# Performance work log

Hardware: AMD Instinct MI355X
Metric: run time of the kernel (lower is better)

The kernel has to match this reference:

```python
import jax, jax.numpy as jnp
import numpy as np

D_MODEL = 1024
NUM_HEADS = 16
D_K = D_MODEL // NUM_HEADS


def setup_inputs() -> dict:
    key = jax.random.key(0)
    ks = jax.random.split(key, 11)
    B, S, D = 2, 2048, D_MODEL
    s = 1.0 / np.sqrt(D)  # torch Linear default init scale
    inp = {
        'query': jax.random.normal(ks[0], (B, S, D), jnp.float32),
        'key': jax.random.normal(ks[1], (B, S, D), jnp.float32),
        'value': jax.random.normal(ks[2], (B, S, D), jnp.float32),
        'Wq': jax.random.uniform(ks[3], (D, D), jnp.float32, -s, s),
        'bq': jax.random.uniform(ks[4], (D,), jnp.float32, -s, s),
        'Wk': jax.random.uniform(ks[5], (D, D), jnp.float32, -s, s),
        'bk': jax.random.uniform(ks[6], (D,), jnp.float32, -s, s),
        'Wv': jax.random.uniform(ks[7], (D, D), jnp.float32, -s, s),
        'bv': jax.random.uniform(ks[8], (D,), jnp.float32, -s, s),
        'Wo': jax.random.uniform(ks[9], (D, D), jnp.float32, -s, s),
        'bo': jax.random.uniform(ks[10], (D,), jnp.float32, -s, s),
    }
    return inp


def reference(query, key, value, Wq, bq, Wk, bk, Wv, bv, Wo, bo):
    B, S, D = query.shape
    H, dk = NUM_HEADS, D_K
    # Linear projections (torch Linear: x @ W.T + b), split into heads -> [B,H,S,dk]
    Q = (query @ Wq.T + bq).reshape(B, S, H, dk).transpose(0, 2, 1, 3)
    K = (key @ Wk.T + bk).reshape(B, S, H, dk).transpose(0, 2, 1, 3)
    V = (value @ Wv.T + bv).reshape(B, S, H, dk).transpose(0, 2, 1, 3)
    scale = jnp.sqrt(jnp.asarray(dk, query.dtype))
    scores = jnp.einsum('bhqd,bhkd->bhqk', Q, K) / scale  # [B,H,S,S]
    attn = jax.nn.softmax(scores, axis=-1)
    ctx = jnp.einsum('bhqk,bhkd->bhqd', attn, V)  # [B,H,S,dk]
    ctx = ctx.transpose(0, 2, 1, 3).reshape(B, S, D)
    return ctx @ Wo.T + bo
```

## Files before the change

kernel.cpp:

```cpp
#include <hip/hip_runtime.h>

#define SEQ 2048
#define DM  1024
#define NH  16
#define DK  64
#define BATCH 2
#define MROWS (BATCH * SEQ)
#define PPITCH 72

typedef __attribute__((ext_vector_type(8))) short bf16x8;
typedef __attribute__((ext_vector_type(4))) float f32x4;

__device__ __forceinline__ float bf2f(unsigned short u) {
    union { unsigned int i; float f; } v;
    v.i = ((unsigned int)u) << 16;
    return v.f;
}

__device__ __forceinline__ unsigned short f2bf(float f) {
    union { float f; unsigned int i; } v;
    v.f = f;
    unsigned int r = v.i + 0x7FFFu + ((v.i >> 16) & 1u);
    return (unsigned short)(r >> 16);
}

__device__ __forceinline__ uint4 pack8(float4 x, float4 y) {
    uint4 r;
    r.x = (unsigned)f2bf(x.x) | ((unsigned)f2bf(x.y) << 16);
    r.y = (unsigned)f2bf(x.z) | ((unsigned)f2bf(x.w) << 16);
    r.z = (unsigned)f2bf(y.x) | ((unsigned)f2bf(y.y) << 16);
    r.w = (unsigned)f2bf(y.z) | ((unsigned)f2bf(y.w) << 16);
    return r;
}

__device__ __forceinline__ void gll16(const void* g, void* l) {
    __builtin_amdgcn_global_load_lds(
        (const __attribute__((address_space(1))) unsigned int*)g,
        (__attribute__((address_space(3))) unsigned int*)l, 16, 0, 0);
}

__global__ void detect_dtype(const unsigned short* __restrict__ q,
                             unsigned int* __restrict__ flag) {
    const int lane = threadIdx.x;
    unsigned short u = q[lane * 2];
    int e = (u >> 7) & 0xFF;
    int hit = (e >= 100 && e <= 135) ? 1 : 0;
    unsigned long long m = __ballot(hit);
    if (lane == 0) *flag = (__popcll(m) >= 48) ? 0u : 1u;
}

#define CVT_TOTAL 16781312u
struct CvtArgs {
    const void* src[11];
    unsigned short* dst[11];
};

__global__ __launch_bounds__(256) void convert_all(CvtArgs a,
                                                   const unsigned int* __restrict__ flagp) {
    const unsigned int f = *flagp;
    const size_t e0 = ((size_t)blockIdx.x * 256 + threadIdx.x) * 8;
    if (e0 >= CVT_TOTAL) return;
    const unsigned int cum[12] = {0u, 4194304u, 8388608u, 12582912u, 13631488u,
                                  14680064u, 15728640u, 16777216u, 16778240u,
                                  16779264u, 16780288u, 16781312u};
    int r = 0;
    #pragma unroll
    for (int i = 1; i < 11; ++i) r += (e0 >= cum[i]) ? 1 : 0;
    const size_t local = e0 - cum[r];
    if (f) {
        const float* s = (const float*)a.src[r] + local;
        float4 x = *(const float4*)s;
        float4 y = *(const float4*)(s + 4);
        *(uint4*)(a.dst[r] + local) = pack8(x, y);
    } else {
        *(uint4*)(a.dst[r] + local) =
            *(const uint4*)((const unsigned short*)a.src[r] + local);
    }
}

__device__ __forceinline__ void gemm_core(
    const unsigned short* __restrict__ A, const unsigned short* __restrict__ W,
    const unsigned short* __restrict__ bias, void* __restrict__ C, int cMode)
{
    __shared__ unsigned short Al[128 * 64];
    __shared__ unsigned short Bl[128 * 64];

    const int tid  = threadIdx.x;
    const int w    = tid >> 6;
    const int lane = tid & 63;
    const int lo   = lane & 15;
    const int quad = lane >> 4;
    const int wr   = w >> 1;
    const int wc   = w & 1;
    const int bm   = blockIdx.y * 128;
    const int bn   = blockIdx.x * 128;

    const int r8  = lane >> 3;
    const int csw = ((lane ^ r8) & 7) * 8;
    const unsigned short* gA = A + (size_t)(bm + w * 32 + r8) * DM + csw;
    const unsigned short* gB = W + (size_t)(bn + w * 32 + r8) * DM + csw;
    unsigned short* lA = &Al[(w * 32) * 64];
    unsigned short* lB = &Bl[(w * 32) * 64];

    f32x4 acc[4][4];
    #pragma unroll
    for (int i = 0; i < 4; ++i)
        #pragma unroll
        for (int n = 0; n < 4; ++n) acc[i][n] = (f32x4){0.f, 0.f, 0.f, 0.f};

    const int swz = (lo & 7);

    for (int k0 = 0; k0 < DM; k0 += 64) {
        __syncthreads();
        #pragma unroll
        for (int j = 0; j < 4; ++j) {
            gll16(gA + (size_t)j * 8 * DM + k0, lA + j * 8 * 64);
            gll16(gB + (size_t)j * 8 * DM + k0, lB + j * 8 * 64);
        }
        __syncthreads();

        #pragma unroll
        for (int kc = 0; kc < 2; ++kc) {
            bf16x8 af[4], bfr[4];
            #pragma unroll
            for (int i = 0; i < 4; ++i)
                af[i] = *(const bf16x8*)&Al[(wr * 64 + i * 16 + lo) * 64 +
                                            (((kc * 4 + quad) ^ swz) * 8)];
            #pragma unroll
            for (int n = 0; n < 4; ++n)
                bfr[n] = *(const bf16x8*)&Bl[(wc * 64 + n * 16 + lo) * 64 +
                                             (((kc * 4 + quad) ^ swz) * 8)];
            #pragma unroll
            for (int i = 0; i < 4; ++i)
                #pragma unroll
                for (int n = 0; n < 4; ++n)
                    acc[i][n] = __builtin_amdgcn_mfma_f32_16x16x32_bf16(af[i], bfr[n], acc[i][n], 0, 0, 0);
        }
    }

    float bj[4];
    #pragma unroll
    for (int n = 0; n < 4; ++n)
        bj[n] = bf2f(bias[bn + wc * 64 + n * 16 + lo]);

    if (cMode == 2) {
        #pragma unroll
        for (int i = 0; i < 4; ++i)
            #pragma unroll
            for (int n = 0; n < 4; ++n) {
                const int row0 = bm + wr * 64 + i * 16 + quad * 4;
                const int col  = bn + wc * 64 + n * 16 + lo;
                ushort4 cv;
                cv.x = f2bf(acc[i][n][0] + bj[n]);
                cv.y = f2bf(acc[i][n][1] + bj[n]);
                cv.z = f2bf(acc[i][n][2] + bj[n]);
                cv.w = f2bf(acc[i][n][3] + bj[n]);
                const size_t off = ((size_t)((row0 >> 11) * 16 + (col >> 6)) * 64
                                    + (col & 63)) * 2048 + (row0 & 2047);
                *(ushort4*)((unsigned short*)C + off) = cv;
            }
    } else {
        #pragma unroll
        for (int i = 0; i < 4; ++i)
            #pragma unroll
            for (int n = 0; n < 4; ++n)
                #pragma unroll
                for (int r = 0; r < 4; ++r) {
                    const int row = bm + wr * 64 + i * 16 + quad * 4 + r;
                    const size_t off = (size_t)row * DM + bn + wc * 64 + n * 16 + lo;
                    const float vv = acc[i][n][r] + bj[n];
                    if (cMode == 1) ((float*)C)[off] = vv;
                    else            ((unsigned short*)C)[off] = f2bf(vv);
                }
    }
}

__global__ __launch_bounds__(256) void gemm_qkv(
    const unsigned short* __restrict__ qa, const unsigned short* __restrict__ ka,
    const unsigned short* __restrict__ va,
    const unsigned short* __restrict__ wq, const unsigned short* __restrict__ wk,
    const unsigned short* __restrict__ wv,
    const unsigned short* __restrict__ bq, const unsigned short* __restrict__ bk,
    const unsigned short* __restrict__ bv,
    unsigned short* __restrict__ oq, unsigned short* __restrict__ ok,
    unsigned short* __restrict__ ovT)
{
    if (blockIdx.z == 0)      gemm_core(qa, wq, bq, oq, 0);
    else if (blockIdx.z == 1) gemm_core(ka, wk, bk, ok, 0);
    else                      gemm_core(va, wv, bv, ovT, 2);
}

__global__ __launch_bounds__(256) void gemm_out(
    const unsigned short* __restrict__ A, const unsigned short* __restrict__ W,
    const unsigned short* __restrict__ B, void* __restrict__ C,
    const unsigned int* __restrict__ flagp)
{
    gemm_core(A, W, B, C, (int)*flagp);
}

__global__ __launch_bounds__(256) void attn_mfma2(
    const unsigned short* __restrict__ Q,
    const unsigned short* __restrict__ K,
    const unsigned short* __restrict__ VT,
    unsigned short* __restrict__ CTX)
{
    __shared__ unsigned short Kl[64 * 64];
    __shared__ unsigned short Vl[64 * 64];
    __shared__ unsigned short Pl[4][2][16 * PPITCH];

    const int tid  = threadIdx.x;
    const int w    = tid >> 6;
    const int lane = tid & 63;
    const int lo   = lane & 15;
    const int quad = lane >> 4;
    const int bh = blockIdx.y;
    const int b  = bh >> 4;
    const int h  = bh & 15;
    const int q0 = blockIdx.x * 128 + w * 32;

    bf16x8 aq[2][2];
    #pragma unroll
    for (int f = 0; f < 2; ++f)
        #pragma unroll
        for (int c = 0; c < 2; ++c)
            aq[f][c] = *(const bf16x8*)(Q + (size_t)(b * SEQ + q0 + f * 16 + lo) * DM
                                        + h * 64 + c * 32 + quad * 8);

    f32x4 o[2][4];
    #pragma unroll
    for (int f = 0; f < 2; ++f)
        #pragma unroll
        for (int dt = 0; dt < 4; ++dt) o[f][dt] = (f32x4){0.f, 0.f, 0.f, 0.f};
    float lsum[2] = {0.f, 0.f};

    const int r8  = lane >> 3;
    const int csw = ((lane ^ r8) & 7) * 8;
    const int swz = lo & 7;
    const unsigned short* Kg = K + (size_t)b * SEQ * DM + h * 64;
    const unsigned short* Vg = VT + (size_t)bh * 64 * 2048;

    for (int j0 = 0; j0 < SEQ; j0 += 64) {
        __syncthreads();
        #pragma unroll
        for (int j = 0; j < 2; ++j) {
            gll16(Kg + (size_t)(j0 + w * 16 + j * 8 + r8) * DM + csw,
                  &Kl[(w * 16 + j * 8) * 64]);
            gll16(Vg + (size_t)(w * 16 + j * 8 + r8) * 2048 + j0 + csw,
                  &Vl[(w * 16 + j * 8) * 64]);
        }
        __syncthreads();

        f32x4 st[4][2];
        #pragma unroll
        for (int kt = 0; kt < 4; ++kt) {
            bf16x8 ak0 = *(const bf16x8*)&Kl[(kt * 16 + lo) * 64 + ((quad ^ swz) * 8)];
            bf16x8 ak1 = *(const bf16x8*)&Kl[(kt * 16 + lo) * 64 + (((4 + quad) ^ swz) * 8)];
            #pragma unroll
            for (int f = 0; f < 2; ++f) {
                f32x4 c = (f32x4){0.f, 0.f, 0.f, 0.f};
                c = __builtin_amdgcn_mfma_f32_16x16x32_bf16(ak0, aq[f][0], c, 0, 0, 0);
                c = __builtin_amdgcn_mfma_f32_16x16x32_bf16(ak1, aq[f][1], c, 0, 0, 0);
                st[kt][f] = c;
            }
        }

        #pragma unroll
        for (int f = 0; f < 2; ++f) {
            #pragma unroll
            for (int kt = 0; kt < 4; ++kt)
                #pragma unroll
                for (int r = 0; r < 4; ++r) {
                    const float p = __expf(st[kt][f][r] * 0.125f);
                    lsum[f] += p;
                    Pl[w][f][lo * PPITCH + kt * 16 + quad * 4 + r] = f2bf(p);
                }
        }
        bf16x8 ap[2][2];
        #pragma unroll
        for (int f = 0; f < 2; ++f)
            #pragma unroll
            for (int c = 0; c < 2; ++c)
                ap[f][c] = *(const bf16x8*)&Pl[w][f][lo * PPITCH + c * 32 + quad * 8];

        #pragma unroll
        for (int dt = 0; dt < 4; ++dt) {
            bf16x8 bv0 = *(const bf16x8*)&Vl[(dt * 16 + lo) * 64 + ((quad ^ swz) * 8)];
            bf16x8 bv1 = *(const bf16x8*)&Vl[(dt * 16 + lo) * 64 + (((4 + quad) ^ swz) * 8)];
            #pragma unroll
            for (int f = 0; f < 2; ++f) {
                o[f][dt] = __builtin_amdgcn_mfma_f32_16x16x32_bf16(ap[f][0], bv0, o[f][dt], 0, 0, 0);
                o[f][dt] = __builtin_amdgcn_mfma_f32_16x16x32_bf16(ap[f][1], bv1, o[f][dt], 0, 0, 0);
            }
        }
    }

    #pragma unroll
    for (int f = 0; f < 2; ++f) {
        lsum[f] += __shfl_xor(lsum[f], 16);
        lsum[f] += __shfl_xor(lsum[f], 32);
    }
    #pragma unroll
    for (int f = 0; f < 2; ++f)
        #pragma unroll
        for (int r = 0; r < 4; ++r) {
            const float lq  = __shfl(lsum[f], quad * 4 + r);
            const float inv = 1.0f / lq;
            const size_t base = (size_t)(b * SEQ + q0 + f * 16 + quad * 4 + r) * DM
                                + h * 64 + lo;
            #pragma unroll
            for (int dt = 0; dt < 4; ++dt)
                CTX[base + dt * 16] = f2bf(o[f][dt][r] * inv);
        }
}

extern "C" void kernel_launch(void* const* d_in, const int* in_sizes, int n_in,
                              void* d_out, int out_size, void* d_ws, size_t ws_size,
                              hipStream_t stream) {
    const size_t E4 = 4194304, E1 = 1048576;
    unsigned short* qb  = (unsigned short*)d_ws;
    unsigned short* kb  = qb  + E4;
    unsigned short* vb  = kb  + E4;
    unsigned short* wqb = vb  + E4;
    unsigned short* wkb = wqb + E1;
    unsigned short* wvb = wkb + E1;
    unsigned short* wob = wvb + E1;
    unsigned short* bqb = wob + E1;
    unsigned short* bkb = bqb + 1024;
    unsigned short* bvb = bkb + 1024;
    unsigned short* bob = bvb + 1024;
    unsigned short* wsQ = bob + 1024;
    unsigned short* wsK = wsQ + E4;
    unsigned short* wsVt = wsK + E4;
    unsigned int*  flag = (unsigned int*)(wsVt + E4);
    unsigned short* wsC = qb;

    detect_dtype<<<1, 64, 0, stream>>>((const unsigned short*)d_in[0], flag);

    CvtArgs ca;
    ca.src[0] = d_in[0];  ca.dst[0] = qb;
    ca.src[1] = d_in[1];  ca.dst[1] = kb;
    ca.src[2] = d_in[2];  ca.dst[2] = vb;
    ca.src[3] = d_in[3];  ca.dst[3] = wqb;
    ca.src[4] = d_in[5];  ca.dst[4] = wkb;
    ca.src[5] = d_in[7];  ca.dst[5] = wvb;
    ca.src[6] = d_in[9];  ca.dst[6] = wob;
    ca.src[7] = d_in[4];  ca.dst[7] = bqb;
    ca.src[8] = d_in[6];  ca.dst[8] = bkb;
    ca.src[9] = d_in[8];  ca.dst[9] = bvb;
    ca.src[10] = d_in[10]; ca.dst[10] = bob;
    convert_all<<<(CVT_TOTAL / 8 + 255) / 256, 256, 0, stream>>>(ca, flag);

    dim3 gq(DM / 128, MROWS / 128, 3);
    gemm_qkv<<<gq, 256, 0, stream>>>(qb, kb, vb, wqb, wkb, wvb,
                                     bqb, bkb, bvb, wsQ, wsK, wsVt);

    dim3 ga(SEQ / 128, BATCH * NH);
    attn_mfma2<<<ga, 256, 0, stream>>>(wsQ, wsK, wsVt, wsC);

    dim3 go(DM / 128, MROWS / 128);
    gemm_out<<<go, 256, 0, stream>>>(wsC, wob, bob, d_out, flag);
}
```

Before: 250.7 us.

## Shrink GEMM tile to 64x128, fold softmax scale into Wq/bq, vectorize P stores

The projection GEMMs now use 64x128 tiles, with each wave owning a 64x32 slice, and launch_bounds asks for 4 blocks per SM. This doubles the grid so more blocks fill the CUs and lowers register pressure. The 1/sqrt(dk)=0.125 scale is pre-applied to Wq and bq in the conversion kernel, which drops a multiply per score in attention. The P tile is written to shared memory as ushort4 instead of scalar stores. Smaller tiles reduce operand reuse and increase global/L2 traffic, and pre-scaling in bf16 is exact only because the factor is a power of two.

```diff
diff --git a/kernel.cpp b/kernel.cpp
--- a/kernel.cpp
+++ b/kernel.cpp
@@ -67,14 +67,24 @@
     #pragma unroll
     for (int i = 1; i < 11; ++i) r += (e0 >= cum[i]) ? 1 : 0;
     const size_t local = e0 - cum[r];
+    const float sc = (r == 3 || r == 7) ? 0.125f : 1.0f;
     if (f) {
         const float* s = (const float*)a.src[r] + local;
         float4 x = *(const float4*)s;
         float4 y = *(const float4*)(s + 4);
+        x.x *= sc; x.y *= sc; x.z *= sc; x.w *= sc;
+        y.x *= sc; y.y *= sc; y.z *= sc; y.w *= sc;
         *(uint4*)(a.dst[r] + local) = pack8(x, y);
     } else {
-        *(uint4*)(a.dst[r] + local) =
-            *(const uint4*)((const unsigned short*)a.src[r] + local);
+        const unsigned short* s = (const unsigned short*)a.src[r] + local;
+        if (sc != 1.0f) {
+            unsigned short o[8];
+            #pragma unroll
+            for (int i = 0; i < 8; ++i) o[i] = f2bf(bf2f(s[i]) * sc);
+            *(uint4*)(a.dst[r] + local) = *(const uint4*)o;
+        } else {
+            *(uint4*)(a.dst[r] + local) = *(const uint4*)s;
+        }
     }
 }
 
@@ -82,7 +92,7 @@
     const unsigned short* __restrict__ A, const unsigned short* __restrict__ W,
     const unsigned short* __restrict__ bias, void* __restrict__ C, int cMode)
 {
-    __shared__ unsigned short Al[128 * 64];
+    __shared__ unsigned short Al[64 * 64];
     __shared__ unsigned short Bl[128 * 64];
 
     const int tid  = threadIdx.x;
@@ -90,66 +100,65 @@
     const int lane = tid & 63;
     const int lo   = lane & 15;
     const int quad = lane >> 4;
-    const int wr   = w >> 1;
-    const int wc   = w & 1;
-    const int bm   = blockIdx.y * 128;
+    const int bm   = blockIdx.y * 64;
     const int bn   = blockIdx.x * 128;
 
     const int r8  = lane >> 3;
     const int csw = ((lane ^ r8) & 7) * 8;
-    const unsigned short* gA = A + (size_t)(bm + w * 32 + r8) * DM + csw;
+    const unsigned short* gA = A + (size_t)(bm + w * 16 + r8) * DM + csw;
     const unsigned short* gB = W + (size_t)(bn + w * 32 + r8) * DM + csw;
-    unsigned short* lA = &Al[(w * 32) * 64];
+    unsigned short* lA = &Al[(w * 16) * 64];
     unsigned short* lB = &Bl[(w * 32) * 64];
 
-    f32x4 acc[4][4];
+    f32x4 acc[4][2];
     #pragma unroll
     for (int i = 0; i < 4; ++i)
         #pragma unroll
-        for (int n = 0; n < 4; ++n) acc[i][n] = (f32x4){0.f, 0.f, 0.f, 0.f};
+        for (int n = 0; n < 2; ++n) acc[i][n] = (f32x4){0.f, 0.f, 0.f, 0.f};
 
     const int swz = (lo & 7);
 
     for (int k0 = 0; k0 < DM; k0 += 64) {
         __syncthreads();
         #pragma unroll
-        for (int j = 0; j < 4; ++j) {
+        for (int j = 0; j < 2; ++j)
             gll16(gA + (size_t)j * 8 * DM + k0, lA + j * 8 * 64);
+        #pragma unroll
+        for (int j = 0; j < 4; ++j)
             gll16(gB + (size_t)j * 8 * DM + k0, lB + j * 8 * 64);
-        }
         __syncthreads();
 
         #pragma unroll
         for (int kc = 0; kc < 2; ++kc) {
-            bf16x8 af[4], bfr[4];
+            bf16x8 af[4], bfr[2];
             #pragma unroll
             for (int i = 0; i < 4; ++i)
-                af[i] = *(const bf16x8*)&Al[(wr * 64 + i * 16 + lo) * 64 +
+                af[i] = *(const bf16x8*)&Al[(i * 16 + lo) * 64 +
                                             (((kc * 4 + quad) ^ swz) * 8)];
             #pragma unroll
-            for (int n = 0; n < 4; ++n)
-                bfr[n] = *(const bf16x8*)&Bl[(wc * 64 + n * 16 + lo) * 64 +
+            for (int n = 0; n < 2; ++n)
+                bfr[n] = *(const bf16x8*)&Bl[(w * 32 + n * 16 + lo) * 64 +
                                              (((kc * 4 + quad) ^ swz) * 8)];
             #pragma unroll
             for (int i = 0; i < 4; ++i)
                 #pragma unroll
-                for (int n = 0; n < 4; ++n)
+                for (int n = 0; n < 2; ++n)
                     acc[i][n] = __builtin_amdgcn_mfma_f32_16x16x32_bf16(af[i], bfr[n], acc[i][n], 0, 0, 0);
         }
     }
 
-    float bj[4];
-    #pragma unroll
-    for (int n = 0; n < 4; ++n)
-        bj[n] = bf2f(bias[bn + wc * 64 + n * 16 + lo]);
+    float bj[2];
+    #pragma unroll
+    for (int n = 0; n < 2; ++n)
+        bj[n] = bf2f(bias[bn + w * 32 + n * 16 + lo]);
 
     if (cMode == 2) {
         #pragma unroll
         for (int i = 0; i < 4; ++i)
             #pragma unroll
-            for (int n = 0; n < 4; ++n) {
-                const int row0 = bm + wr * 64 + i * 16 + quad * 4;
-                const int col  = bn + wc * 64 + n * 16 + lo;
+            for (int n = 0; n < 2; ++n) {
+                const int row0 = bm + i * 16 + quad * 4;
+                const int col  = bn + w * 32 + n * 16 + lo;
                 ushort4 cv;
                 cv.x = f2bf(acc[i][n][0] + bj[n]);
                 cv.y = f2bf(acc[i][n][1] + bj[n]);
@@ -163,11 +172,11 @@
         #pragma unroll
         for (int i = 0; i < 4; ++i)
             #pragma unroll
-            for (int n = 0; n < 4; ++n)
+            for (int n = 0; n < 2; ++n)
                 #pragma unroll
                 for (int r = 0; r < 4; ++r) {
-                    const int row = bm + wr * 64 + i * 16 + quad * 4 + r;
-                    const size_t off = (size_t)row * DM + bn + wc * 64 + n * 16 + lo;
+                    const int row = bm + i * 16 + quad * 4 + r;
+                    const size_t off = (size_t)row * DM + bn + w * 32 + n * 16 + lo;
                     const float vv = acc[i][n][r] + bj[n];
                     if (cMode == 1) ((float*)C)[off] = vv;
                     else            ((unsigned short*)C)[off] = f2bf(vv);
@@ -175,7 +184,7 @@
     }
 }
 
-__global__ __launch_bounds__(256) void gemm_qkv(
+__global__ __launch_bounds__(256, 4) void gemm_qkv(
     const unsigned short* __restrict__ qa, const unsigned short* __restrict__ ka,
     const unsigned short* __restrict__ va,
     const unsigned short* __restrict__ wq, const unsigned short* __restrict__ wk,
@@ -190,7 +199,7 @@
     else                      gemm_core(va, wv, bv, ovT, 2);
 }
 
-__global__ __launch_bounds__(256) void gemm_out(
+__global__ __launch_bounds__(256, 4) void gemm_out(
     const unsigned short* __restrict__ A, const unsigned short* __restrict__ W,
     const unsigned short* __restrict__ B, void* __restrict__ C,
     const unsigned int* __restrict__ flagp)
@@ -265,16 +274,16 @@
         }
 
         #pragma unroll
-        for (int f = 0; f < 2; ++f) {
-            #pragma unroll
-            for (int kt = 0; kt < 4; ++kt)
-                #pragma unroll
-                for (int r = 0; r < 4; ++r) {
-                    const float p = __expf(st[kt][f][r] * 0.125f);
-                    lsum[f] += p;
-                    Pl[w][f][lo * PPITCH + kt * 16 + quad * 4 + r] = f2bf(p);
-                }
-        }
+        for (int f = 0; f < 2; ++f)
+            #pragma unroll
+            for (int kt = 0; kt < 4; ++kt) {
+                float p0 = __expf(st[kt][f][0]), p1 = __expf(st[kt][f][1]);
+                float p2 = __expf(st[kt][f][2]), p3 = __expf(st[kt][f][3]);
+                lsum[f] += (p0 + p1) + (p2 + p3);
+                ushort4 pv;
+                pv.x = f2bf(p0); pv.y = f2bf(p1); pv.z = f2bf(p2); pv.w = f2bf(p3);
+                *(ushort4*)&Pl[w][f][lo * PPITCH + kt * 16 + quad * 4] = pv;
+            }
         bf16x8 ap[2][2];
         #pragma unroll
         for (int f = 0; f < 2; ++f)
@@ -350,13 +359,13 @@
     ca.src[10] = d_in[10]; ca.dst[10] = bob;
     convert_all<<<(CVT_TOTAL / 8 + 255) / 256, 256, 0, stream>>>(ca, flag);
 
-    dim3 gq(DM / 128, MROWS / 128, 3);
+    dim3 gq(DM / 128, MROWS / 64, 3);
     gemm_qkv<<<gq, 256, 0, stream>>>(qb, kb, vb, wqb, wkb, wvb,
                                      bqb, bkb, bvb, wsQ, wsK, wsVt);
 
     dim3 ga(SEQ / 128, BATCH * NH);
     attn_mfma2<<<ga, 256, 0, stream>>>(wsQ, wsK, wsVt, wsC);
 
-    dim3 go(DM / 128, MROWS / 128);
+    dim3 go(DM / 128, MROWS / 64);
     gemm_out<<<go, 256, 0, stream>>>(wsC, wob, bob, d_out, flag);
 }
```

New measurement: 244.0 us. -2.7%, faster.
